# Optimization experiments

Hardware: AMD Instinct MI355X
Metric: run time of the kernel (lower is better)

Reference implementation:

```python
import jax, jax.numpy as jnp
import numpy as np

B, L, C = 4, 1024, 768
H = 12
D = C // H  # head_dim = 64


def setup_inputs() -> dict:
    key = jax.random.key(0)
    k_x, k_qkv, k_pw, k_pb = jax.random.split(key, 4)
    x = jax.random.normal(k_x, (B, L, C), dtype=jnp.float32)
    # torch nn.Linear(C, 3C, bias=False): weight [3C, C]
    w_qkv = jax.random.normal(k_qkv, (3 * C, C), dtype=jnp.float32) * (1.0 / np.sqrt(C))
    # torch nn.Linear(C, C): weight [C, C], bias [C]
    w_proj = jax.random.normal(k_pw, (C, C), dtype=jnp.float32) * (1.0 / np.sqrt(C))
    b_proj = jax.random.normal(k_pb, (C,), dtype=jnp.float32) * 0.01
    return {"x": x, "w_qkv": w_qkv, "w_proj": w_proj, "b_proj": b_proj}


def reference(x, w_qkv, w_proj, b_proj):
    scale = D ** (-0.5)
    # qkv: [B, L, 3C] -> [3, B, H, L, D]
    qkv = jnp.einsum('blc,fc->blf', x, w_qkv)
    qkv = qkv.reshape(B, L, 3, H, D).transpose(2, 0, 3, 1, 4)
    q, k, v = qkv[0], qkv[1], qkv[2]
    # attention scores [B, H, L, L], materialized (returned by the module)
    attn = jnp.einsum('bhld,bhmd->bhlm', q, k) * scale
    attn_score = jax.nn.softmax(attn, axis=-1)
    # dropout_p = 0.0 -> identity
    out = jnp.einsum('bhlm,bhmd->bhld', attn_score, v)
    out = out.transpose(0, 2, 1, 3).reshape(B, L, C)
    out = jnp.einsum('blc,fc->blf', out, w_proj) + b_proj
    return (out, attn_score)
```

## Files before the change

kernel.cpp:

```cpp
#include <hip/hip_runtime.h>
#include <hip/hip_bf16.h>
#include <stdint.h>


typedef __attribute__((ext_vector_type(8))) short short8;
typedef __attribute__((ext_vector_type(4))) float floatx4;

#define MFMA16(A_, B_, C_) __builtin_amdgcn_mfma_f32_16x16x32_bf16((A_), (B_), (C_), 0, 0, 0)

__device__ __forceinline__ unsigned short f2bf(float f) {
  unsigned u = __builtin_bit_cast(unsigned, f);
  u += 0x7FFFu + ((u >> 16) & 1u);
  return (unsigned short)(u >> 16);
}
__device__ __forceinline__ float bf2f(unsigned short u) {
  return __builtin_bit_cast(float, (unsigned)u << 16);
}

__global__ __launch_bounds__(256) void cast3_kernel(const float* __restrict__ x,
                                                    const float* __restrict__ wq,
                                                    const float* __restrict__ wp,
                                                    unsigned short* __restrict__ dst) {
  const int NX = 3145728, NWQ = 1769472;
  int i = (blockIdx.x * 256 + threadIdx.x) * 4;
  const float* src;
  int off;
  if (i < NX) { src = x; off = i; }
  else if (i < NX + NWQ) { src = wq; off = i - NX; }
  else { src = wp; off = i - NX - NWQ; }
  float4 v = *(const float4*)(src + off);
  ushort4 o;
  o.x = f2bf(v.x); o.y = f2bf(v.y); o.z = f2bf(v.z); o.w = f2bf(v.w);
  *(ushort4*)(dst + i) = o;
}

template <int EPI, int BN>
__global__ __launch_bounds__(256) void gemm_bt(
    const unsigned short* __restrict__ A, const unsigned short* __restrict__ Bm,
    const float* __restrict__ bias,
    unsigned short* __restrict__ q_ws, unsigned short* __restrict__ k_ws,
    unsigned short* __restrict__ vt_ws, float* __restrict__ Cout,
    int M, int N, int K) {
  constexpr int NJ = BN / 32;
  constexpr int QN = BN / 2;
  __shared__ __align__(16) unsigned short Al[2][128 * 32];
  __shared__ __align__(16) unsigned short Bl[2][BN * 32];
  const int tid = threadIdx.x;
  const int lane = tid & 63, wave = tid >> 6;
  const int q = lane >> 4, lm = lane & 15;
  const int wm = wave >> 1, wn = wave & 1;
  const int m0 = blockIdx.y * 128, n0 = blockIdx.x * BN;

  floatx4 acc[4][NJ];
#pragma unroll
  for (int i = 0; i < 4; ++i)
#pragma unroll
    for (int j = 0; j < NJ; ++j) acc[i][j] = (floatx4){0.f, 0.f, 0.f, 0.f};

  auto stage = [&](int k0, int buf) {
#pragma unroll
    for (int it = 0; it < 2; ++it) {
      int idx = tid + it * 256;
      int row = idx >> 2, ch = idx & 3;
      const unsigned short* ga = A + (size_t)(m0 + row) * K + k0 + ch * 8;
      __builtin_amdgcn_global_load_lds(
          (const __attribute__((address_space(1))) unsigned int*)ga,
          (__attribute__((address_space(3))) unsigned int*)(&Al[buf][0] + idx * 8), 16, 0, 0);
    }
#pragma unroll
    for (int it = 0; it < BN / 64; ++it) {
      int idx = tid + it * 256;
      int row = idx >> 2, ch = idx & 3;
      const unsigned short* gb = Bm + (size_t)(n0 + row) * K + k0 + ch * 8;
      __builtin_amdgcn_global_load_lds(
          (const __attribute__((address_space(1))) unsigned int*)gb,
          (__attribute__((address_space(3))) unsigned int*)(&Bl[buf][0] + idx * 8), 16, 0, 0);
    }
  };

  stage(0, 0);
  __syncthreads();
  int cur = 0;
  for (int k0 = 0; k0 < K; k0 += 32) {
    if (k0 + 32 < K) stage(k0 + 32, cur ^ 1);
    short8 af[4], bfr[NJ];
#pragma unroll
    for (int t = 0; t < 4; ++t)
      af[t] = *(const short8*)(&Al[cur][0] + (wm * 64 + t * 16 + lm) * 32 + q * 8);
#pragma unroll
    for (int t = 0; t < NJ; ++t)
      bfr[t] = *(const short8*)(&Bl[cur][0] + (wn * QN + t * 16 + lm) * 32 + q * 8);
#pragma unroll
    for (int i = 0; i < 4; ++i)
#pragma unroll
      for (int j = 0; j < NJ; ++j) acc[i][j] = MFMA16(af[i], bfr[j], acc[i][j]);
    __syncthreads();
    cur ^= 1;
  }

  if (EPI == 0) {
#pragma unroll
    for (int i = 0; i < 4; ++i) {
      int mb = m0 + wm * 64 + i * 16 + q * 4;
#pragma unroll
      for (int j = 0; j < NJ; ++j) {
        int n = n0 + wn * QN + j * 16 + lm;
        int which = n / 768;
        int r = n - which * 768;
        int h = r >> 6, d = r & 63;
        if (which == 2) {
          int b = mb >> 10, l = mb & 1023;
          ushort4 pk;
          pk.x = f2bf(acc[i][j][0]);
          pk.y = f2bf(acc[i][j][1]);
          pk.z = f2bf(acc[i][j][2]);
          pk.w = f2bf(acc[i][j][3]);
          *(ushort4*)(vt_ws + (size_t)((b * 12 + h) * 64 + d) * 1024 + l) = pk;
        } else {
          unsigned short* dst = (which == 0) ? q_ws : k_ws;
          float sc = (which == 0) ? 0.125f : 1.0f;
#pragma unroll
          for (int rg = 0; rg < 4; ++rg) {
            int m = mb + rg;
            int b = m >> 10, l = m & 1023;
            dst[(size_t)((b * 12 + h) * 1024 + l) * 64 + d] = f2bf(acc[i][j][rg] * sc);
          }
        }
      }
    }
  } else {
#pragma unroll
    for (int i = 0; i < 4; ++i) {
      int mb = m0 + wm * 64 + i * 16 + q * 4;
#pragma unroll
      for (int j = 0; j < NJ; ++j) {
        int n = n0 + wn * QN + j * 16 + lm;
        float bv = bias[n];
#pragma unroll
        for (int rg = 0; rg < 4; ++rg) {
          int m = mb + rg;
          Cout[(size_t)m * N + n] = acc[i][j][rg] + bv;
        }
      }
    }
  }
}

__global__ __launch_bounds__(256) void attn_mfma(
    const unsigned short* __restrict__ q_ws, const unsigned short* __restrict__ k_ws,
    const unsigned short* __restrict__ vt_ws, unsigned short* __restrict__ attn_o,
    float* __restrict__ out1) {
  constexpr int L = 1024, SW = 1032;
  constexpr float LOG2E = 1.44269504f;
  __shared__ __align__(16) unsigned short S[16 * SW];
  __shared__ float stats[2][4][16];
  const int flat = blockIdx.x;
  const int swz = (flat & 7) * 384 + (flat >> 3);
  const int bh = swz >> 6, b = bh / 12, h = bh % 12;
  const int l0 = (swz & 63) * 16;
  const int tid = threadIdx.x, lane = tid & 63, wave = tid >> 6;
  const int q = lane >> 4, lm = lane & 15;

  const size_t qk_base = (size_t)bh * L * 64;

  const unsigned short* qr = q_ws + qk_base + (size_t)(l0 + lm) * 64;
  short8 bq0 = *(const short8*)(qr + q * 8);
  short8 bq1 = *(const short8*)(qr + 32 + q * 8);

  floatx4 acc[16];
  __builtin_amdgcn_s_setprio(1);
#pragma unroll
  for (int ct = 0; ct < 16; ++ct) {
    const unsigned short* kr = k_ws + qk_base + (size_t)((wave * 16 + ct) * 16 + lm) * 64;
    short8 a0 = *(const short8*)(kr + q * 8);
    short8 a1 = *(const short8*)(kr + 32 + q * 8);
    floatx4 c = (floatx4){0.f, 0.f, 0.f, 0.f};
    c = MFMA16(a0, bq0, c);
    c = MFMA16(a1, bq1, c);
    acc[ct] = c;
  }
  __builtin_amdgcn_s_setprio(0);

  float mloc = -1e30f;
#pragma unroll
  for (int ct = 0; ct < 16; ++ct)
#pragma unroll
    for (int rg = 0; rg < 4; ++rg) mloc = fmaxf(mloc, acc[ct][rg]);
  mloc = fmaxf(mloc, __shfl_xor(mloc, 16));
  mloc = fmaxf(mloc, __shfl_xor(mloc, 32));

  float ssum = 0.f;
#pragma unroll
  for (int ct = 0; ct < 16; ++ct) {
#pragma unroll
    for (int rg = 0; rg < 4; ++rg) {
      float e = exp2f((acc[ct][rg] - mloc) * LOG2E);
      acc[ct][rg] = e;
      ssum += e;
    }
  }
  ssum += __shfl_xor(ssum, 16);
  ssum += __shfl_xor(ssum, 32);
  if (lane < 16) {
    stats[0][wave][lane] = mloc;
    stats[1][wave][lane] = ssum;
  }
  __syncthreads();

  float m0_ = stats[0][0][lm], m1_ = stats[0][1][lm];
  float m2_ = stats[0][2][lm], m3_ = stats[0][3][lm];
  float m = fmaxf(fmaxf(m0_, m1_), fmaxf(m2_, m3_));
  float sum = stats[1][0][lm] * exp2f((m0_ - m) * LOG2E)
            + stats[1][1][lm] * exp2f((m1_ - m) * LOG2E)
            + stats[1][2][lm] * exp2f((m2_ - m) * LOG2E)
            + stats[1][3][lm] * exp2f((m3_ - m) * LOG2E);
  float wscale = exp2f((mloc - m) * LOG2E) / sum;

  float* orow = out1 + (size_t)bh * L * L + (size_t)(l0 + lm) * L + wave * 256 + q * 4;
  unsigned short* srow = S + lm * SW + wave * 256 + q * 4;
#pragma unroll
  for (int ct = 0; ct < 16; ++ct) {
    float p0 = acc[ct][0] * wscale, p1 = acc[ct][1] * wscale;
    float p2 = acc[ct][2] * wscale, p3 = acc[ct][3] * wscale;
    ushort4 pk;
    pk.x = f2bf(p0); pk.y = f2bf(p1); pk.z = f2bf(p2); pk.w = f2bf(p3);
    *(ushort4*)(srow + ct * 16) = pk;
    float4 pv;
    pv.x = p0; pv.y = p1; pv.z = p2; pv.w = p3;
    *(float4*)(orow + ct * 16) = pv;
  }
  __syncthreads();

  {
    floatx4 pacc = (floatx4){0.f, 0.f, 0.f, 0.f};
    const unsigned short* vr = vt_ws + (size_t)(bh * 64 + wave * 16 + lm) * 1024;
    __builtin_amdgcn_s_setprio(1);
#pragma unroll 4
    for (int ks = 0; ks < 32; ++ks) {
      short8 af = *(const short8*)(S + lm * SW + ks * 32 + q * 8);
      short8 bv = *(const short8*)(vr + ks * 32 + q * 8);
      pacc = MFMA16(af, bv, pacc);
    }
    __builtin_amdgcn_s_setprio(0);
#pragma unroll
    for (int rg = 0; rg < 4; ++rg) {
      int row = q * 4 + rg;
      attn_o[(size_t)(b * 1024 + l0 + row) * 768 + h * 64 + wave * 16 + lm] = f2bf(pacc[rg]);
    }
  }
}

extern "C" void kernel_launch(void* const* d_in, const int* in_sizes, int n_in,
                              void* d_out, int out_size, void* d_ws, size_t ws_size,
                              hipStream_t stream) {
  const float* x      = (const float*)d_in[0];
  const float* w_qkv  = (const float*)d_in[1];
  const float* w_proj = (const float*)d_in[2];
  const float* b_proj = (const float*)d_in[3];

  float* out0 = (float*)d_out;
  float* out1 = out0 + (size_t)4096 * 768;

  const size_t NX = (size_t)4096 * 768;
  const size_t NWQ = (size_t)2304 * 768;
  const size_t NWP = (size_t)768 * 768;
  const size_t NQ = (size_t)48 * 1024 * 64;

  unsigned short* x_bf   = (unsigned short*)d_ws;
  unsigned short* wq_bf  = x_bf + NX;
  unsigned short* wp_bf  = wq_bf + NWQ;
  unsigned short* q_ws   = wp_bf + NWP;
  unsigned short* k_ws   = q_ws + NQ;
  unsigned short* vt_ws  = k_ws + NQ;
  unsigned short* attn_o = vt_ws + NQ;

  cast3_kernel<<<dim3((NX + NWQ + NWP) / 1024), dim3(256), 0, stream>>>(x, w_qkv, w_proj, x_bf);

  gemm_bt<0, 128><<<dim3(2304 / 128, 4096 / 128), dim3(256), 0, stream>>>(
      x_bf, wq_bf, nullptr, q_ws, k_ws, vt_ws, nullptr, 4096, 2304, 768);

  attn_mfma<<<dim3(3072), dim3(256), 0, stream>>>(q_ws, k_ws, vt_ws, attn_o, out1);

  gemm_bt<1, 64><<<dim3(768 / 64, 4096 / 128), dim3(256), 0, stream>>>(
      attn_o, wp_bf, b_proj, nullptr, nullptr, nullptr, out0, 4096, 768, 768);
}
```

Baseline: 339.0 us.

## Swizzle GEMM blocks per XCD, use nontemporal stores, split PV accumulators

Both GEMM launches become a 1D grid whose block index is remapped so that consecutive tiles land on the same XCD (8-way chunking), aiming for better L2 reuse of A/B tiles. The large fp32 attention-score writes and the projection output writes use nontemporal stores to avoid polluting the cache. The PV MFMA loop is split into two independent accumulators to break the dependency chain between successive MFMAs. Together these add index arithmetic and an extra vector add, and rely on the grid sizes dividing evenly by 8.

```diff
diff --git a/kernel.cpp b/kernel.cpp
--- a/kernel.cpp
+++ b/kernel.cpp
@@ -40,7 +40,7 @@
     const float* __restrict__ bias,
     unsigned short* __restrict__ q_ws, unsigned short* __restrict__ k_ws,
     unsigned short* __restrict__ vt_ws, float* __restrict__ Cout,
-    int M, int N, int K) {
+    int M, int N, int K, int nbx, int chunk) {
   constexpr int NJ = BN / 32;
   constexpr int QN = BN / 2;
   __shared__ __align__(16) unsigned short Al[2][128 * 32];
@@ -49,7 +49,9 @@
   const int lane = tid & 63, wave = tid >> 6;
   const int q = lane >> 4, lm = lane & 15;
   const int wm = wave >> 1, wn = wave & 1;
-  const int m0 = blockIdx.y * 128, n0 = blockIdx.x * BN;
+  const int flat = blockIdx.x;
+  const int swz = (flat & 7) * chunk + (flat >> 3);
+  const int m0 = (swz / nbx) * 128, n0 = (swz % nbx) * BN;
 
   floatx4 acc[4][NJ];
 #pragma unroll
@@ -139,7 +141,7 @@
 #pragma unroll
         for (int rg = 0; rg < 4; ++rg) {
           int m = mb + rg;
-          Cout[(size_t)m * N + n] = acc[i][j][rg] + bv;
+          __builtin_nontemporal_store(acc[i][j][rg] + bv, Cout + (size_t)m * N + n);
         }
       }
     }
@@ -225,23 +227,28 @@
     ushort4 pk;
     pk.x = f2bf(p0); pk.y = f2bf(p1); pk.z = f2bf(p2); pk.w = f2bf(p3);
     *(ushort4*)(srow + ct * 16) = pk;
-    float4 pv;
-    pv.x = p0; pv.y = p1; pv.z = p2; pv.w = p3;
-    *(float4*)(orow + ct * 16) = pv;
+    floatx4 pv = (floatx4){p0, p1, p2, p3};
+    __builtin_nontemporal_store(pv, (floatx4*)(orow + ct * 16));
   }
   __syncthreads();
 
   {
-    floatx4 pacc = (floatx4){0.f, 0.f, 0.f, 0.f};
+    floatx4 pacc0 = (floatx4){0.f, 0.f, 0.f, 0.f};
+    floatx4 pacc1 = (floatx4){0.f, 0.f, 0.f, 0.f};
     const unsigned short* vr = vt_ws + (size_t)(bh * 64 + wave * 16 + lm) * 1024;
+    const unsigned short* sbase = S + lm * SW;
     __builtin_amdgcn_s_setprio(1);
 #pragma unroll 4
-    for (int ks = 0; ks < 32; ++ks) {
-      short8 af = *(const short8*)(S + lm * SW + ks * 32 + q * 8);
-      short8 bv = *(const short8*)(vr + ks * 32 + q * 8);
-      pacc = MFMA16(af, bv, pacc);
+    for (int ks = 0; ks < 32; ks += 2) {
+      short8 af0 = *(const short8*)(sbase + ks * 32 + q * 8);
+      short8 bv0 = *(const short8*)(vr + ks * 32 + q * 8);
+      pacc0 = MFMA16(af0, bv0, pacc0);
+      short8 af1 = *(const short8*)(sbase + (ks + 1) * 32 + q * 8);
+      short8 bv1 = *(const short8*)(vr + (ks + 1) * 32 + q * 8);
+      pacc1 = MFMA16(af1, bv1, pacc1);
     }
     __builtin_amdgcn_s_setprio(0);
+    floatx4 pacc = pacc0 + pacc1;
 #pragma unroll
     for (int rg = 0; rg < 4; ++rg) {
       int row = q * 4 + rg;
@@ -276,11 +283,11 @@
 
   cast3_kernel<<<dim3((NX + NWQ + NWP) / 1024), dim3(256), 0, stream>>>(x, w_qkv, w_proj, x_bf);
 
-  gemm_bt<0, 128><<<dim3(2304 / 128, 4096 / 128), dim3(256), 0, stream>>>(
-      x_bf, wq_bf, nullptr, q_ws, k_ws, vt_ws, nullptr, 4096, 2304, 768);
+  gemm_bt<0, 128><<<dim3(576), dim3(256), 0, stream>>>(
+      x_bf, wq_bf, nullptr, q_ws, k_ws, vt_ws, nullptr, 4096, 2304, 768, 18, 72);
 
   attn_mfma<<<dim3(3072), dim3(256), 0, stream>>>(q_ws, k_ws, vt_ws, attn_o, out1);
 
-  gemm_bt<1, 64><<<dim3(768 / 64, 4096 / 128), dim3(256), 0, stream>>>(
-      attn_o, wp_bf, b_proj, nullptr, nullptr, nullptr, out0, 4096, 768, 768);
-}
+  gemm_bt<1, 64><<<dim3(384), dim3(256), 0, stream>>>(
+      attn_o, wp_bf, b_proj, nullptr, nullptr, nullptr, out0, 4096, 768, 768, 12, 48);
+}
```

Result: no change. 340.6 us (+0.5%).
